# Kernel tuning notes

Hardware: AMD Instinct MI355X
Metric: run time of the kernel (lower is better)

## Reference

```python
import jax, jax.numpy as jnp
import numpy as np

DIM = 1024
NUM_HEADS = 16
HEAD_DIM = DIM // NUM_HEADS
SCALE = HEAD_DIM ** -0.5
NEG = -1e9


def setup_inputs() -> dict:
    key = jax.random.key(0)
    ks = jax.random.split(key, 10)
    B, N, M, C = 8, 1024, 1024, DIM
    q = jax.random.normal(ks[0], (B, N, C), jnp.float32)
    k = jax.random.normal(ks[1], (B, M, C), jnp.float32)
    v = jax.random.normal(ks[2], (B, M, C), jnp.float32)
    mask = jax.random.randint(ks[3], (B, N), 0, 2, jnp.int32)
    target_mask = jax.random.randint(ks[4], (B, N, M), 0, 2, jnp.int32)
    Wq = jax.random.normal(ks[5], (C, C), jnp.float32) * 0.02
    Wk = jax.random.normal(ks[6], (C, C), jnp.float32) * 0.02
    Wv = jax.random.normal(ks[7], (C, C), jnp.float32) * 0.02
    Wo = jax.random.normal(ks[8], (C, C), jnp.float32) * 0.02
    bo = jnp.zeros((C,), jnp.float32)
    return {"q": q, "k": k, "v": v, "mask": mask, "target_mask": target_mask,
            "Wq": Wq, "Wk": Wk, "Wv": Wv, "Wo": Wo, "bo": bo}


def reference(q, k, v, mask, target_mask, Wq, Wk, Wv, Wo, bo):
    B, N, C = q.shape
    M = k.shape[1]
    H, D = NUM_HEADS, HEAD_DIM
    qh = (q @ Wq).reshape(B, N, H, D)
    kh = (k @ Wk).reshape(B, M, H, D)
    vh = (v @ Wv).reshape(B, M, H, D)
    attn = jnp.einsum('bnhd,bmhd->bhnm', qh, kh) * SCALE  # (B,H,N,M)
    # self-attn key mask (B,N) -> broadcast over queries (requires N==M as in original)
    attn = jnp.where(mask[:, None, None, :] == 0, NEG, attn)
    # cross-attn mask (B,N,M) -> broadcast over heads
    attn = jnp.where(target_mask[:, None, :, :] == 0, NEG, attn)
    attn = jax.nn.softmax(attn, axis=-1)
    x = jnp.einsum('bhnm,bmhd->bnhd', attn, vh).reshape(B, N, C)
    return x @ Wo + bo
```

## Files before the change

kernel.cpp:

```cpp
#include <hip/hip_runtime.h>
#include <hip/hip_bf16.h>

#define DEV __device__ __forceinline__

typedef __attribute__((ext_vector_type(8))) short bf16x8;
typedef __attribute__((ext_vector_type(4))) float f32x4;
typedef unsigned int u32;
typedef unsigned long long u64;

DEV short f2bf(float f) {
  union { float f; u32 u; } x; x.f = f;
  u32 r = x.u + 0x7fffu + ((x.u >> 16) & 1u);
  return (short)(r >> 16);
}

DEV void gload_lds16(const void* g, void* l) {
  __builtin_amdgcn_global_load_lds(
      (const __attribute__((address_space(1))) u32*)g,
      (__attribute__((address_space(3))) u32*)l, 16, 0, 0);
}

DEV void stage_t128(const char* base, int ktb, char* lds, int w, int lane) {
  int r8 = lane >> 3;
  int csw = ((lane & 7) ^ r8) << 4;
#pragma unroll
  for (int i = 0; i < 4; ++i) {
    int c = w * 4 + i;
    gload_lds16(base + (size_t)(c * 8 + r8) * 2048 + ktb + csw, lds + c * 1024);
  }
}

DEV bf16x8 frag(const short* L, int row, int col) {
  return *(const bf16x8*)&L[row * 64 + (col ^ ((row & 7) << 3))];
}

__global__ __launch_bounds__(256) void aconv(const float* __restrict__ q,
    const float* __restrict__ k, const float* __restrict__ v,
    short* __restrict__ qb, short* __restrict__ kb, short* __restrict__ vb) {
  const float* src; short* dst;
  if (blockIdx.z == 0)      { src = q; dst = qb; }
  else if (blockIdx.z == 1) { src = k; dst = kb; }
  else                      { src = v; dst = vb; }
  size_t i = ((size_t)blockIdx.x * 256 + threadIdx.x) * 8;
  float4 f0 = *(const float4*)(src + i);
  float4 f1 = *(const float4*)(src + i + 4);
  bf16x8 o;
  o[0] = f2bf(f0.x); o[1] = f2bf(f0.y); o[2] = f2bf(f0.z); o[3] = f2bf(f0.w);
  o[4] = f2bf(f1.x); o[5] = f2bf(f1.y); o[6] = f2bf(f1.z); o[7] = f2bf(f1.w);
  *(bf16x8*)(dst + i) = o;
}

__global__ __launch_bounds__(256) void pack_mask(const int* __restrict__ mask,
                                                 const int* __restrict__ tmask,
                                                 u64* __restrict__ pk) {
  int bn = blockIdx.x;
  int b = bn >> 10;
  int t = threadIdx.x, w = t >> 6, lane = t & 63;
  const int* tr = tmask + (size_t)bn * 1024;
  const int* mr = mask + b * 1024;
#pragma unroll
  for (int it = 0; it < 4; ++it) {
    int m = it * 256 + w * 64 + lane;
    bool on = (mr[m] != 0) && (tr[m] != 0);
    u64 bits = __ballot(on);
    if (lane == 0) pk[(size_t)bn * 16 + it * 4 + w] = bits;
  }
}

__global__ __launch_bounds__(256) void wconv4(const float* __restrict__ W0,
    const float* __restrict__ W1, const float* __restrict__ W2,
    const float* __restrict__ W3, short* __restrict__ WtAll) {
  const float* W = blockIdx.z == 0 ? W0 : blockIdx.z == 1 ? W1
                 : blockIdx.z == 2 ? W2 : W3;
  short* Wt = WtAll + (size_t)blockIdx.z * 1024 * 1024;
  __shared__ short tile[64][65];
  int k0 = blockIdx.x * 64, n0 = blockIdx.y * 64;
  int t = threadIdx.x;
  int r = t >> 2, c = (t & 3) * 16;
  const float* src = W + (size_t)(k0 + r) * 1024 + n0 + c;
#pragma unroll
  for (int i = 0; i < 16; i += 4) {
    float4 f = *(const float4*)(src + i);
    tile[r][c + i + 0] = f2bf(f.x);
    tile[r][c + i + 1] = f2bf(f.y);
    tile[r][c + i + 2] = f2bf(f.z);
    tile[r][c + i + 3] = f2bf(f.w);
  }
  __syncthreads();
  bf16x8 v0, v1;
#pragma unroll
  for (int i = 0; i < 8; ++i) v0[i] = tile[c + i][r];
#pragma unroll
  for (int i = 0; i < 8; ++i) v1[i] = tile[c + 8 + i][r];
  short* dst = Wt + (size_t)(n0 + r) * 1024 + k0 + c;
  *(bf16x8*)(dst) = v0;
  *(bf16x8*)(dst + 8) = v1;
}

__global__ __launch_bounds__(256) void vtrans(const short* __restrict__ vh,
                                              short* __restrict__ vht) {
  __shared__ short tile[64][65];
  int m0 = blockIdx.x * 64;
  int bh = blockIdx.y;
  int t = threadIdx.x;
  int r = t >> 2, c = (t & 3) * 16;
  const short* src = vh + ((size_t)bh * 1024 + m0 + r) * 64 + c;
  bf16x8 a0 = *(const bf16x8*)(src);
  bf16x8 a1 = *(const bf16x8*)(src + 8);
#pragma unroll
  for (int i = 0; i < 8; ++i) tile[r][c + i] = a0[i];
#pragma unroll
  for (int i = 0; i < 8; ++i) tile[r][c + 8 + i] = a1[i];
  __syncthreads();
  bf16x8 v0, v1;
#pragma unroll
  for (int i = 0; i < 8; ++i) v0[i] = tile[c + i][r];
#pragma unroll
  for (int i = 0; i < 8; ++i) v1[i] = tile[c + 8 + i][r];
  short* dst = vht + ((size_t)bh * 64 + r) * 1024 + m0 + c;
  *(bf16x8*)dst = v0;
  *(bf16x8*)(dst + 8) = v1;
}

#define QSCALE 0.18033688011112042f

__global__ __launch_bounds__(256, 2) void gemm_qkv(
    const short* __restrict__ qb, const short* __restrict__ kb, const short* __restrict__ vb,
    const short* __restrict__ WtAll,
    short* __restrict__ qh, short* __restrict__ kh, short* __restrict__ vh) {
  int flat = blockIdx.z * 512 + blockIdx.y * 8 + blockIdx.x;
  int nid = (flat & 7) * 192 + (flat >> 3);
  int zz = nid >> 9;
  int rr = nid & 511;
  int bm = (rr >> 3) * 128, bn = (rr & 7) * 128;

  const short* A; short* Ch; float cs;
  if (zz == 0)      { A = qb; Ch = qh; cs = QSCALE; }
  else if (zz == 1) { A = kb; Ch = kh; cs = 1.0f; }
  else              { A = vb; Ch = vh; cs = 1.0f; }
  const short* Wt = WtAll + (size_t)zz * 1024 * 1024;

  __shared__ __align__(16) short As[128 * 64];
  __shared__ __align__(16) short Bs[128 * 64];

  int tid = threadIdx.x;
  int lane = tid & 63, w = tid >> 6;
  int wm = w >> 1, wn = w & 1;
  int lr = lane & 15, lg = lane >> 4;

  const f32x4 fz = {0.f, 0.f, 0.f, 0.f};
  f32x4 acc[4][4];
#pragma unroll
  for (int i = 0; i < 4; ++i)
#pragma unroll
    for (int j = 0; j < 4; ++j) acc[i][j] = fz;

  const char* abase = (const char*)A + (size_t)bm * 2048;
  const char* bbase = (const char*)Wt + (size_t)bn * 2048;

  for (int ktb = 0; ktb < 2048; ktb += 128) {
    stage_t128(abase, ktb, (char*)As, w, lane);
    stage_t128(bbase, ktb, (char*)Bs, w, lane);
    __syncthreads();
#pragma unroll
    for (int ks = 0; ks < 2; ++ks) {
      bf16x8 af[4], bfr[4];
#pragma unroll
      for (int mi = 0; mi < 4; ++mi)
        af[mi] = frag(As, wm * 64 + mi * 16 + lr, ks * 32 + lg * 8);
#pragma unroll
      for (int ni = 0; ni < 4; ++ni)
        bfr[ni] = frag(Bs, wn * 64 + ni * 16 + lr, ks * 32 + lg * 8);
#pragma unroll
      for (int mi = 0; mi < 4; ++mi)
#pragma unroll
        for (int ni = 0; ni < 4; ++ni)
          acc[mi][ni] = __builtin_amdgcn_mfma_f32_16x16x32_bf16(af[mi], bfr[ni], acc[mi][ni], 0, 0, 0);
    }
    __syncthreads();
  }
#pragma unroll
  for (int mi = 0; mi < 4; ++mi)
#pragma unroll
    for (int ni = 0; ni < 4; ++ni) {
      int ccol = bn + wn * 64 + ni * 16 + lr;
      int h = ccol >> 6, d = ccol & 63;
#pragma unroll
      for (int j = 0; j < 4; ++j) {
        int r = bm + wm * 64 + mi * 16 + lg * 4 + j;
        int bb = r >> 10, n = r & 1023;
        Ch[(((size_t)bb * 16 + h) * 1024 + n) * 64 + d] = f2bf(acc[mi][ni][j] * cs);
      }
    }
}

DEV void stage_kv(const char* kbase, const char* vbase, int kv0,
                  short* Ksb, short* Vsb, int w, int lane) {
#pragma unroll
  for (int i = 0; i < 2; ++i) {
    int c = w * 2 + i;
    int row = (lane >> 3);
    int colb = ((lane & 7) ^ row) << 4;
    gload_lds16(kbase + (size_t)(kv0 + c * 8 + row) * 128 + colb, (char*)Ksb + c * 1024);
    gload_lds16(vbase + (size_t)(c * 8 + row) * 2048 + kv0 * 2 + colb, (char*)Vsb + c * 1024);
  }
}

__global__ __launch_bounds__(256, 2) void attn(
    const short* __restrict__ qh, const short* __restrict__ kh, const short* __restrict__ vht,
    const u64* __restrict__ pk, short* __restrict__ x) {
  __shared__ __align__(16) short Ks[2][4096];
  __shared__ __align__(16) short Vs[2][4096];
  __shared__ __align__(16) short Ps[8192];

  int flat = blockIdx.y * 8 + blockIdx.x;
  int nid = (flat & 7) * 128 + (flat >> 3);
  int bh = nid >> 3, qt = nid & 7;
  int b = bh >> 4;
  int tid = threadIdx.x, lane = tid & 63, w = tid >> 6;
  int lr = lane & 15, lg = lane >> 4;

  bf16x8 qa[2][2];
  {
    const short* qb2 = qh + ((size_t)bh * 1024 + qt * 128 + w * 32) * 64;
#pragma unroll
    for (int mi = 0; mi < 2; ++mi)
#pragma unroll
      for (int ks = 0; ks < 2; ++ks)
        qa[mi][ks] = *(const bf16x8*)(qb2 + (mi * 16 + lr) * 64 + ks * 32 + lg * 8);
  }

  const f32x4 fz = {0.f, 0.f, 0.f, 0.f};
  f32x4 o[2][4];
  float psum[2][4];
#pragma unroll
  for (int mi = 0; mi < 2; ++mi)
#pragma unroll
    for (int j = 0; j < 4; ++j) psum[mi][j] = 0.f;
#pragma unroll
  for (int mi = 0; mi < 2; ++mi)
#pragma unroll
    for (int nd = 0; nd < 4; ++nd) o[mi][nd] = fz;

  const char* kbase = (const char*)(kh + (size_t)bh * 65536);
  const char* vbase = (const char*)(vht + (size_t)bh * 65536);
  const u64* pkb = pk + ((size_t)b * 1024 + qt * 128) * 16;

  stage_kv(kbase, vbase, 0, Ks[0], Vs[0], w, lane);
  __syncthreads();
  int cur = 0;

  for (int t = 0; t < 16; ++t) {
    if (t < 15) stage_kv(kbase, vbase, (t + 1) * 64, Ks[cur ^ 1], Vs[cur ^ 1], w, lane);

    u64 pw[2][4];
#pragma unroll
    for (int mi = 0; mi < 2; ++mi)
#pragma unroll
      for (int j = 0; j < 4; ++j)
        pw[mi][j] = pkb[(w * 32 + mi * 16 + lg * 4 + j) * 16 + t];

    f32x4 s[2][4];
#pragma unroll
    for (int mi = 0; mi < 2; ++mi)
#pragma unroll
      for (int ni = 0; ni < 4; ++ni) s[mi][ni] = fz;
#pragma unroll
    for (int ks = 0; ks < 2; ++ks) {
      bf16x8 kb2[4];
#pragma unroll
      for (int ni = 0; ni < 4; ++ni)
        kb2[ni] = *(const bf16x8*)&Ks[cur][(ni * 16 + lr) * 64 + ((ks * 32 + lg * 8) ^ ((lr & 7) << 3))];
#pragma unroll
      for (int mi = 0; mi < 2; ++mi)
#pragma unroll
        for (int ni = 0; ni < 4; ++ni)
          s[mi][ni] = __builtin_amdgcn_mfma_f32_16x16x32_bf16(qa[mi][ks], kb2[ni], s[mi][ni], 0, 0, 0);
    }

#pragma unroll
    for (int mi = 0; mi < 2; ++mi)
#pragma unroll
      for (int j = 0; j < 4; ++j) {
        u32 lo = (u32)pw[mi][j], hi = (u32)(pw[mi][j] >> 32);
        float rs = 0.f;
#pragma unroll
        for (int ni = 0; ni < 4; ++ni) {
          u32 bit = ((ni < 2 ? lo : hi) >> ((ni & 1) * 16 + lr)) & 1u;
          float e = __builtin_amdgcn_exp2f(s[mi][ni][j]);
          float p = bit ? e : 0.f;
          s[mi][ni][j] = p;
          rs += p;
        }
        psum[mi][j] += rs;
      }

#pragma unroll
    for (int mi = 0; mi < 2; ++mi)
#pragma unroll
      for (int j = 0; j < 4; ++j) {
        int r = w * 32 + mi * 16 + lg * 4 + j;
        int sw = (r & 7) << 3;
#pragma unroll
        for (int ni = 0; ni < 4; ++ni)
          Ps[r * 64 + ((ni * 16 + lr) ^ sw)] = f2bf(s[mi][ni][j]);
      }

#pragma unroll
    for (int ks = 0; ks < 2; ++ks) {
      bf16x8 pa[2], vb2[4];
#pragma unroll
      for (int mi = 0; mi < 2; ++mi)
        pa[mi] = *(const bf16x8*)&Ps[(w * 32 + mi * 16 + lr) * 64 + ((ks * 32 + lg * 8) ^ ((lr & 7) << 3))];
#pragma unroll
      for (int nd = 0; nd < 4; ++nd)
        vb2[nd] = *(const bf16x8*)&Vs[cur][(nd * 16 + lr) * 64 + ((ks * 32 + lg * 8) ^ ((lr & 7) << 3))];
#pragma unroll
      for (int mi = 0; mi < 2; ++mi)
#pragma unroll
        for (int nd = 0; nd < 4; ++nd)
          o[mi][nd] = __builtin_amdgcn_mfma_f32_16x16x32_bf16(pa[mi], vb2[nd], o[mi][nd], 0, 0, 0);
    }
    __syncthreads();
    cur ^= 1;
  }

  short* xb = x + ((size_t)b * 1024) * 1024 + (bh & 15) * 64;
#pragma unroll
  for (int mi = 0; mi < 2; ++mi)
#pragma unroll
    for (int j = 0; j < 4; ++j) {
      float rs = psum[mi][j];
#pragma unroll
      for (int dd = 1; dd < 16; dd <<= 1) rs += __shfl_xor(rs, dd, 64);
      float inv = rs > 0.f ? 1.0f / rs : 0.f;
      int qg = qt * 128 + w * 32 + mi * 16 + lg * 4 + j;
#pragma unroll
      for (int nd = 0; nd < 4; ++nd) {
        int d = nd * 16 + lr;
        xb[(size_t)qg * 1024 + d] = f2bf(o[mi][nd][j] * inv);
      }
    }
}

__global__ __launch_bounds__(256, 2) void gemm_out(
    const short* __restrict__ X, const short* __restrict__ Wot,
    const float* __restrict__ bo, float* __restrict__ out) {
  int flat = blockIdx.y * 8 + blockIdx.x;
  int nid = (flat & 7) * 64 + (flat >> 3);
  int bm = (nid >> 3) * 128, bn = (nid & 7) * 128;

  __shared__ __align__(16) short As[128 * 64];
  __shared__ __align__(16) short Bs[128 * 64];
  int tid = threadIdx.x, lane = tid & 63, w = tid >> 6;
  int wm = w >> 1, wn = w & 1, lr = lane & 15, lg = lane >> 4;

  const f32x4 fz = {0.f, 0.f, 0.f, 0.f};
  f32x4 acc[4][4];
#pragma unroll
  for (int i = 0; i < 4; ++i)
#pragma unroll
    for (int j = 0; j < 4; ++j) acc[i][j] = fz;

  const char* abase = (const char*)X + (size_t)bm * 2048;
  const char* bbase = (const char*)Wot + (size_t)bn * 2048;

  for (int ktb = 0; ktb < 2048; ktb += 128) {
    stage_t128(abase, ktb, (char*)As, w, lane);
    stage_t128(bbase, ktb, (char*)Bs, w, lane);
    __syncthreads();
#pragma unroll
    for (int ks = 0; ks < 2; ++ks) {
      bf16x8 af[4], bfr[4];
#pragma unroll
      for (int mi = 0; mi < 4; ++mi)
        af[mi] = frag(As, wm * 64 + mi * 16 + lr, ks * 32 + lg * 8);
#pragma unroll
      for (int ni = 0; ni < 4; ++ni)
        bfr[ni] = frag(Bs, wn * 64 + ni * 16 + lr, ks * 32 + lg * 8);
#pragma unroll
      for (int mi = 0; mi < 4; ++mi)
#pragma unroll
        for (int ni = 0; ni < 4; ++ni)
          acc[mi][ni] = __builtin_amdgcn_mfma_f32_16x16x32_bf16(af[mi], bfr[ni], acc[mi][ni], 0, 0, 0);
    }
    __syncthreads();
  }
#pragma unroll
  for (int mi = 0; mi < 4; ++mi)
#pragma unroll
    for (int ni = 0; ni < 4; ++ni) {
      int ccol = bn + wn * 64 + ni * 16 + lr;
      float bias = bo[ccol];
#pragma unroll
      for (int j = 0; j < 4; ++j) {
        int r = bm + wm * 64 + mi * 16 + lg * 4 + j;
        out[(size_t)r * 1024 + ccol] = acc[mi][ni][j] + bias;
      }
    }
}

extern "C" void kernel_launch(void* const* d_in, const int* in_sizes, int n_in,
                              void* d_out, int out_size, void* d_ws, size_t ws_size,
                              hipStream_t stream) {
  const float* q = (const float*)d_in[0];
  const float* k = (const float*)d_in[1];
  const float* v = (const float*)d_in[2];
  const int* mask = (const int*)d_in[3];
  const int* tmask = (const int*)d_in[4];
  const float* Wq = (const float*)d_in[5];
  const float* Wk = (const float*)d_in[6];
  const float* Wv = (const float*)d_in[7];
  const float* Wo = (const float*)d_in[8];
  const float* bo = (const float*)d_in[9];
  float* out = (float*)d_out;

  char* ws = (char*)d_ws;
  const size_t MB = 1u << 20;
  if (ws_size < 73 * MB) return;
  short* WtAll = (short*)(ws + 0 * MB);
  short* qh  = (short*)(ws + 8 * MB);
  short* kh  = (short*)(ws + 24 * MB);
  short* vh  = (short*)(ws + 40 * MB);
  short* vht = (short*)(ws + 56 * MB);
  u64*   pkb = (u64*)(ws + 72 * MB);
  short* x   = (short*)(ws + 40 * MB);
  short* qbA = (short*)d_out;
  short* kbA = (short*)d_out + 8 * 1024 * 1024;
  short* vbA = (short*)(ws + 56 * MB);

  aconv<<<dim3(4096, 1, 3), 256, 0, stream>>>(q, k, v, qbA, kbA, vbA);
  wconv4<<<dim3(16, 16, 4), 256, 0, stream>>>(Wq, Wk, Wv, Wo, WtAll);
  pack_mask<<<dim3(8192), 256, 0, stream>>>(mask, tmask, pkb);

  gemm_qkv<<<dim3(8, 64, 3), 256, 0, stream>>>(qbA, kbA, vbA, WtAll, qh, kh, vh);
  vtrans<<<dim3(16, 128), 256, 0, stream>>>(vh, vht);
  attn<<<dim3(8, 128), 256, 0, stream>>>(qh, kh, vht, pkb, x);
  gemm_out<<<dim3(8, 64), 256, 0, stream>>>(x, WtAll + 3 * 1024 * 1024, bo, out);
}
```

Before: 350.7 us.

## Process two 128-row query tiles per attention block to reuse staged K/V

Each attention block now handles 256 queries (two 128-row sub-tiles) against each staged K/V tile, halving the grid and the total K/V global-to-LDS traffic per query. P is double-buffered in LDS per sub-tile, and s_setprio raises wave priority around the MFMA sections. The bf16 conversion of P is simplified to round-half-up without ties-to-even. This costs more registers (doubled accumulators and Q fragments) and halves the block count (512 blocks), which may reduce occupancy or leave compute units underfilled.

```diff
diff --git a/kernel.cpp b/kernel.cpp
--- a/kernel.cpp
+++ b/kernel.cpp
@@ -211,40 +211,39 @@
     const u64* __restrict__ pk, short* __restrict__ x) {
   __shared__ __align__(16) short Ks[2][4096];
   __shared__ __align__(16) short Vs[2][4096];
-  __shared__ __align__(16) short Ps[8192];
+  __shared__ __align__(16) short Ps[2][8192];
 
   int flat = blockIdx.y * 8 + blockIdx.x;
-  int nid = (flat & 7) * 128 + (flat >> 3);
-  int bh = nid >> 3, qt = nid & 7;
+  int nid = (flat & 7) * 64 + (flat >> 3);
+  int bh = nid >> 2, qp = nid & 3;
   int b = bh >> 4;
   int tid = threadIdx.x, lane = tid & 63, w = tid >> 6;
   int lr = lane & 15, lg = lane >> 4;
 
-  bf16x8 qa[2][2];
-  {
-    const short* qb2 = qh + ((size_t)bh * 1024 + qt * 128 + w * 32) * 64;
+  bf16x8 qa[2][2][2];
+#pragma unroll
+  for (int sub = 0; sub < 2; ++sub) {
+    const short* qb2 = qh + ((size_t)bh * 1024 + qp * 256 + sub * 128 + w * 32) * 64;
 #pragma unroll
     for (int mi = 0; mi < 2; ++mi)
 #pragma unroll
       for (int ks = 0; ks < 2; ++ks)
-        qa[mi][ks] = *(const bf16x8*)(qb2 + (mi * 16 + lr) * 64 + ks * 32 + lg * 8);
+        qa[sub][mi][ks] = *(const bf16x8*)(qb2 + (mi * 16 + lr) * 64 + ks * 32 + lg * 8);
   }
 
   const f32x4 fz = {0.f, 0.f, 0.f, 0.f};
-  f32x4 o[2][4];
-  float psum[2][4];
-#pragma unroll
-  for (int mi = 0; mi < 2; ++mi)
-#pragma unroll
-    for (int j = 0; j < 4; ++j) psum[mi][j] = 0.f;
-#pragma unroll
-  for (int mi = 0; mi < 2; ++mi)
-#pragma unroll
-    for (int nd = 0; nd < 4; ++nd) o[mi][nd] = fz;
+  f32x4 o[2][2][4];
+  float psum[2][2][4];
+#pragma unroll
+  for (int sub = 0; sub < 2; ++sub)
+#pragma unroll
+    for (int mi = 0; mi < 2; ++mi)
+#pragma unroll
+      for (int j = 0; j < 4; ++j) { psum[sub][mi][j] = 0.f; o[sub][mi][j] = fz; }
 
   const char* kbase = (const char*)(kh + (size_t)bh * 65536);
   const char* vbase = (const char*)(vht + (size_t)bh * 65536);
-  const u64* pkb = pk + ((size_t)b * 1024 + qt * 128) * 16;
+  const u64* pkb = pk + ((size_t)b * 1024 + qp * 256) * 16;
 
   stage_kv(kbase, vbase, 0, Ks[0], Vs[0], w, lane);
   __syncthreads();
@@ -253,73 +252,72 @@
   for (int t = 0; t < 16; ++t) {
     if (t < 15) stage_kv(kbase, vbase, (t + 1) * 64, Ks[cur ^ 1], Vs[cur ^ 1], w, lane);
 
-    u64 pw[2][4];
-#pragma unroll
-    for (int mi = 0; mi < 2; ++mi)
-#pragma unroll
-      for (int j = 0; j < 4; ++j)
-        pw[mi][j] = pkb[(w * 32 + mi * 16 + lg * 4 + j) * 16 + t];
-
-    f32x4 s[2][4];
-#pragma unroll
-    for (int mi = 0; mi < 2; ++mi)
-#pragma unroll
-      for (int ni = 0; ni < 4; ++ni) s[mi][ni] = fz;
-#pragma unroll
-    for (int ks = 0; ks < 2; ++ks) {
-      bf16x8 kb2[4];
-#pragma unroll
-      for (int ni = 0; ni < 4; ++ni)
-        kb2[ni] = *(const bf16x8*)&Ks[cur][(ni * 16 + lr) * 64 + ((ks * 32 + lg * 8) ^ ((lr & 7) << 3))];
+#pragma unroll
+    for (int sub = 0; sub < 2; ++sub) {
+      u64 pw[2][4];
 #pragma unroll
       for (int mi = 0; mi < 2; ++mi)
 #pragma unroll
+        for (int j = 0; j < 4; ++j)
+          pw[mi][j] = pkb[(sub * 128 + w * 32 + mi * 16 + lg * 4 + j) * 16 + t];
+
+      f32x4 s[2][4];
+#pragma unroll
+      for (int mi = 0; mi < 2; ++mi)
+#pragma unroll
+        for (int ni = 0; ni < 4; ++ni) s[mi][ni] = fz;
+      __builtin_amdgcn_s_setprio(1);
+#pragma unroll
+      for (int ks = 0; ks < 2; ++ks) {
+        bf16x8 kb2[4];
+#pragma unroll
         for (int ni = 0; ni < 4; ++ni)
-          s[mi][ni] = __builtin_amdgcn_mfma_f32_16x16x32_bf16(qa[mi][ks], kb2[ni], s[mi][ni], 0, 0, 0);
-    }
-
-#pragma unroll
-    for (int mi = 0; mi < 2; ++mi)
-#pragma unroll
-      for (int j = 0; j < 4; ++j) {
-        u32 lo = (u32)pw[mi][j], hi = (u32)(pw[mi][j] >> 32);
-        float rs = 0.f;
-#pragma unroll
-        for (int ni = 0; ni < 4; ++ni) {
-          u32 bit = ((ni < 2 ? lo : hi) >> ((ni & 1) * 16 + lr)) & 1u;
-          float e = __builtin_amdgcn_exp2f(s[mi][ni][j]);
-          float p = bit ? e : 0.f;
-          s[mi][ni][j] = p;
-          rs += p;
+          kb2[ni] = *(const bf16x8*)&Ks[cur][(ni * 16 + lr) * 64 + ((ks * 32 + lg * 8) ^ ((lr & 7) << 3))];
+#pragma unroll
+        for (int mi = 0; mi < 2; ++mi)
+#pragma unroll
+          for (int ni = 0; ni < 4; ++ni)
+            s[mi][ni] = __builtin_amdgcn_mfma_f32_16x16x32_bf16(qa[sub][mi][ks], kb2[ni], s[mi][ni], 0, 0, 0);
+      }
+      __builtin_amdgcn_s_setprio(0);
+
+#pragma unroll
+      for (int mi = 0; mi < 2; ++mi)
+#pragma unroll
+        for (int j = 0; j < 4; ++j) {
+          u32 lo = (u32)pw[mi][j], hi = (u32)(pw[mi][j] >> 32);
+          int r = w * 32 + mi * 16 + lg * 4 + j;
+          int sw = (r & 7) << 3;
+          float rs = 0.f;
+#pragma unroll
+          for (int ni = 0; ni < 4; ++ni) {
+            u32 bit = ((ni < 2 ? lo : hi) >> ((ni & 1) * 16 + lr)) & 1u;
+            float e = __builtin_amdgcn_exp2f(s[mi][ni][j]);
+            float p = bit ? e : 0.f;
+            rs += p;
+            union { float f; u32 u; } cv; cv.f = p;
+            Ps[sub][r * 64 + ((ni * 16 + lr) ^ sw)] = (short)((cv.u + 0x8000u) >> 16);
+          }
+          psum[sub][mi][j] += rs;
         }
-        psum[mi][j] += rs;
+
+      __builtin_amdgcn_s_setprio(1);
+#pragma unroll
+      for (int ks = 0; ks < 2; ++ks) {
+        bf16x8 pa[2], vb2[4];
+#pragma unroll
+        for (int mi = 0; mi < 2; ++mi)
+          pa[mi] = *(const bf16x8*)&Ps[sub][(w * 32 + mi * 16 + lr) * 64 + ((ks * 32 + lg * 8) ^ ((lr & 7) << 3))];
+#pragma unroll
+        for (int nd = 0; nd < 4; ++nd)
+          vb2[nd] = *(const bf16x8*)&Vs[cur][(nd * 16 + lr) * 64 + ((ks * 32 + lg * 8) ^ ((lr & 7) << 3))];
+#pragma unroll
+        for (int mi = 0; mi < 2; ++mi)
+#pragma unroll
+          for (int nd = 0; nd < 4; ++nd)
+            o[sub][mi][nd] = __builtin_amdgcn_mfma_f32_16x16x32_bf16(pa[mi], vb2[nd], o[sub][mi][nd], 0, 0, 0);
       }
-
-#pragma unroll
-    for (int mi = 0; mi < 2; ++mi)
-#pragma unroll
-      for (int j = 0; j < 4; ++j) {
-        int r = w * 32 + mi * 16 + lg * 4 + j;
-        int sw = (r & 7) << 3;
-#pragma unroll
-        for (int ni = 0; ni < 4; ++ni)
-          Ps[r * 64 + ((ni * 16 + lr) ^ sw)] = f2bf(s[mi][ni][j]);
-      }
-
-#pragma unroll
-    for (int ks = 0; ks < 2; ++ks) {
-      bf16x8 pa[2], vb2[4];
-#pragma unroll
-      for (int mi = 0; mi < 2; ++mi)
-        pa[mi] = *(const bf16x8*)&Ps[(w * 32 + mi * 16 + lr) * 64 + ((ks * 32 + lg * 8) ^ ((lr & 7) << 3))];
-#pragma unroll
-      for (int nd = 0; nd < 4; ++nd)
-        vb2[nd] = *(const bf16x8*)&Vs[cur][(nd * 16 + lr) * 64 + ((ks * 32 + lg * 8) ^ ((lr & 7) << 3))];
-#pragma unroll
-      for (int mi = 0; mi < 2; ++mi)
-#pragma unroll
-        for (int nd = 0; nd < 4; ++nd)
-          o[mi][nd] = __builtin_amdgcn_mfma_f32_16x16x32_bf16(pa[mi], vb2[nd], o[mi][nd], 0, 0, 0);
+      __builtin_amdgcn_s_setprio(0);
     }
     __syncthreads();
     cur ^= 1;
@@ -327,20 +325,22 @@
 
   short* xb = x + ((size_t)b * 1024) * 1024 + (bh & 15) * 64;
 #pragma unroll
-  for (int mi = 0; mi < 2; ++mi)
-#pragma unroll
-    for (int j = 0; j < 4; ++j) {
-      float rs = psum[mi][j];
-#pragma unroll
-      for (int dd = 1; dd < 16; dd <<= 1) rs += __shfl_xor(rs, dd, 64);
-      float inv = rs > 0.f ? 1.0f / rs : 0.f;
-      int qg = qt * 128 + w * 32 + mi * 16 + lg * 4 + j;
-#pragma unroll
-      for (int nd = 0; nd < 4; ++nd) {
-        int d = nd * 16 + lr;
-        xb[(size_t)qg * 1024 + d] = f2bf(o[mi][nd][j] * inv);
+  for (int sub = 0; sub < 2; ++sub)
+#pragma unroll
+    for (int mi = 0; mi < 2; ++mi)
+#pragma unroll
+      for (int j = 0; j < 4; ++j) {
+        float rs = psum[sub][mi][j];
+#pragma unroll
+        for (int dd = 1; dd < 16; dd <<= 1) rs += __shfl_xor(rs, dd, 64);
+        float inv = rs > 0.f ? 1.0f / rs : 0.f;
+        int qg = qp * 256 + sub * 128 + w * 32 + mi * 16 + lg * 4 + j;
+#pragma unroll
+        for (int nd = 0; nd < 4; ++nd) {
+          int d = nd * 16 + lr;
+          xb[(size_t)qg * 1024 + d] = f2bf(o[sub][mi][nd][j] * inv);
+        }
       }
-    }
 }
 
 __global__ __launch_bounds__(256, 2) void gemm_out(
@@ -435,6 +435,6 @@
 
   gemm_qkv<<<dim3(8, 64, 3), 256, 0, stream>>>(qbA, kbA, vbA, WtAll, qh, kh, vh);
   vtrans<<<dim3(16, 128), 256, 0, stream>>>(vh, vht);
-  attn<<<dim3(8, 128), 256, 0, stream>>>(qh, kh, vht, pkb, x);
+  attn<<<dim3(8, 64), 256, 0, stream>>>(qh, kh, vht, pkb, x);
   gemm_out<<<dim3(8, 64), 256, 0, stream>>>(x, WtAll + 3 * 1024 * 1024, bo, out);
 }
```

After: 335.9 us. 4.2% less time.
